# Performance work log

Measured on AMD Instinct MI355X. Metric: run time of the kernel, lower is better.

## Reference

```python
import jax, jax.numpy as jnp
import numpy as np

N_SEQ, N_RES, C_M = 1024, 768, 64
NUM_HEAD = 8
HEAD_DIM = C_M // NUM_HEAD  # key_dim == value_dim == 8 per head
LARGE = 1e9
LN_EPS = 1e-5
MEAN_EPS = 1e-10


def setup_inputs() -> dict:
    key = jax.random.key(0)
    ks = jax.random.split(key, 8)
    msa_act = jax.random.normal(ks[0], (N_SEQ, N_RES, C_M), dtype=jnp.float32)
    msa_mask = (jax.random.uniform(ks[1], (N_SEQ, N_RES)) > 0.15).astype(jnp.float32)
    # fan-avg uniform init like VarianceScaling(1.0, 'fan_avg', 'uniform')
    def vs(k, shape, fan_in, fan_out):
        limit = jnp.sqrt(3.0 * 2.0 / (fan_in + fan_out))
        return jax.random.uniform(k, shape, minval=-limit, maxval=limit, dtype=jnp.float32)
    return {
        "msa_act": msa_act,
        "msa_mask": msa_mask,
        "ln_scale": jnp.ones((C_M,), jnp.float32),
        "ln_bias": jnp.zeros((C_M,), jnp.float32),
        "query_w": vs(ks[2], (C_M, NUM_HEAD, HEAD_DIM), C_M, NUM_HEAD * HEAD_DIM),
        "key_w": vs(ks[3], (C_M, HEAD_DIM), C_M, HEAD_DIM),
        "value_w": vs(ks[4], (C_M, HEAD_DIM), C_M, HEAD_DIM),
        "gating_w": jnp.zeros((C_M, NUM_HEAD, HEAD_DIM), jnp.float32),
        "gating_b": jnp.ones((NUM_HEAD, HEAD_DIM), jnp.float32),
        "output_w": vs(ks[5], (NUM_HEAD, HEAD_DIM, C_M), NUM_HEAD * HEAD_DIM, C_M),
        "output_b": jnp.zeros((C_M,), jnp.float32),
    }


def reference(msa_act, msa_mask, ln_scale, ln_bias, query_w, key_w, value_w,
              gating_w, gating_b, output_w, output_b):
    # permute: columns become the batch axis b = N_res
    x = jnp.transpose(msa_act, (1, 0, 2))          # [R, S, C]
    mask = jnp.transpose(msa_mask, (1, 0))[..., None]  # [R, S, 1]

    # LayerNorm over channels
    mu = jnp.mean(x, axis=-1, keepdims=True)
    var = jnp.mean(jnp.square(x - mu), axis=-1, keepdims=True)
    x = (x - mu) * jax.lax.rsqrt(var + LN_EPS) * ln_scale + ln_bias

    # shared (non-per-head) K/V projections
    v = jnp.einsum('bka,ac->bkc', x, value_w)      # [R, S, d]
    k = jnp.einsum('bka,ac->bkc', x, key_w)        # [R, S, d]

    # masked-mean single query per column
    q_avg = jnp.sum(mask * x, axis=1) / (jnp.sum(mask, axis=1) + MEAN_EPS)  # [R, C]
    q = jnp.einsum('ba,ahc->bhc', q_avg, query_w) * (HEAD_DIM ** -0.5)      # [R, H, d]

    bias = LARGE * (mask[:, None, :, 0] - 1.0)     # [R, 1, S]
    logits = jnp.einsum('bhc,bkc->bhk', q, k) + bias
    weights = jax.nn.softmax(logits, axis=-1)      # [R, H, S]
    weighted_avg = jnp.einsum('bhk,bkc->bhc', weights, v)  # [R, H, d]

    # sigmoid gating per (query, head, channel)
    gate = jax.nn.sigmoid(jnp.einsum('bqc,chv->bqhv', x, gating_w) + gating_b)  # [R, S, H, d]
    gated = weighted_avg[:, None] * gate           # [R, S, H, d]
    out = jnp.einsum('bqhc,hco->bqo', gated, output_w) + output_b  # [R, S, C]

    return jnp.transpose(out, (1, 0, 2))           # [S, R, C]
```

## Files before the change

kernel.cpp:

```cpp
#include <hip/hip_runtime.h>
#include <hip/hip_bf16.h>

#define N_S 1024
#define N_R 768
#define LN_EPS 1e-5f
#define MEAN_EPS 1e-10f
#define LARGE_F 1e9f
#define QSCALE 0.35355339059327373f

typedef __attribute__((ext_vector_type(8))) __bf16 bf16x8;
typedef __attribute__((ext_vector_type(4))) float f32x4;

__device__ __forceinline__ float bflo(unsigned u){ union{unsigned v; float f;} x; x.v = u << 16; return x.f; }
__device__ __forceinline__ unsigned short f2b(float f){
  __hip_bfloat16 h = __float2bfloat16(f);
  return *reinterpret_cast<unsigned short*>(&h);
}
__device__ __forceinline__ unsigned pk2(float a, float b){
  return (unsigned)f2b(a) | ((unsigned)f2b(b) << 16);
}
__device__ __forceinline__ bf16x8 ld_frag(const void* p){
  uint4 u = *reinterpret_cast<const uint4*>(p);
  return __builtin_bit_cast(bf16x8, u);
}

__device__ __forceinline__ void weight_prep(int wave, int lane,
    const float* __restrict__ gw, const float* __restrict__ ow, uint4* __restrict__ wsf)
{
  #pragma unroll 1
  for (int rep = 0; rep < 2; rep++) {
    int fi = wave + rep * 4;
    int mf = fi >> 1, ks = fi & 1;
    int g = lane >> 4, c15 = lane & 15;
    union { uint4 u; unsigned short h[8]; } ghi, glo, ohi, olo;
    #pragma unroll
    for (int t = 0; t < 8; t++) {
      int k = ks * 32 + g * 8 + t;
      float gv = gw[k * 64 + mf * 16 + c15];
      unsigned short gh = f2b(gv);
      ghi.h[t] = gh;
      glo.h[t] = f2b(gv - bflo(gh));
      float ov = ow[k * 64 + mf * 16 + c15];
      unsigned short oh = f2b(ov);
      ohi.h[t] = oh;
      olo.h[t] = f2b(ov - bflo(oh));
    }
    wsf[(0 * 8 + fi) * 64 + lane] = ghi.u;
    wsf[(1 * 8 + fi) * 64 + lane] = glo.u;
    wsf[(2 * 8 + fi) * 64 + lane] = ohi.u;
    wsf[(3 * 8 + fi) * 64 + lane] = olo.u;
  }
}

__global__ __launch_bounds__(256, 2) void lnkv_kernel(
    const float* __restrict__ act, const float* __restrict__ mask,
    const float* __restrict__ lns, const float* __restrict__ lnb,
    const float* __restrict__ kw,  const float* __restrict__ vw,
    const float* __restrict__ gw,  const float* __restrict__ ow,
    _Float16* __restrict__ kvws,   float* __restrict__ qpart,
    float* __restrict__ mpart,     uint4* __restrict__ wsf)
{
  __shared__ float redA[4][64];
  __shared__ float redB[4];

  const int tid  = threadIdx.x;
  const int lane = tid & 63;
  const int wave = tid >> 6;
  const int b    = blockIdx.x;

  if (b >= 6144) { weight_prep(wave, lane, gw, ow, wsf); return; }

  const int r  = b >> 3;
  const int sc = b & 7;
  const int s  = sc * 128 + (tid >> 1);
  const int h  = tid & 1;

  float rw[32];
  {
    const float4* rp = reinterpret_cast<const float4*>(
        act + ((size_t)s * N_R + r) * 64 + h * 32);
    #pragma unroll
    for (int i = 0; i < 8; i++) reinterpret_cast<float4*>(rw)[i] = rp[i];
  }
  float m = mask[(size_t)s * N_R + r];

  float sum = 0.f, ss = 0.f;
  #pragma unroll
  for (int i = 0; i < 32; i++) { sum += rw[i]; ss += rw[i] * rw[i]; }
  sum += __shfl_xor(sum, 1);
  ss  += __shfl_xor(ss, 1);
  float mu  = sum * (1.f / 64.f);
  float rsd = rsqrtf(ss * (1.f / 64.f) - mu * mu + LN_EPS);

  float kacc[8], vacc[8];
  #pragma unroll
  for (int d = 0; d < 8; d++) { kacc[d] = 0.f; vacc[d] = 0.f; }
  #pragma unroll
  for (int i = 0; i < 32; i++) {
    int c = h * 32 + i;
    float xn = fmaf((rw[i] - mu) * rsd, lns[c], lnb[c]);
    rw[i] = m * xn;
    #pragma unroll
    for (int d = 0; d < 8; d++) {
      kacc[d] = fmaf(xn, kw[c * 8 + d], kacc[d]);
      vacc[d] = fmaf(xn, vw[c * 8 + d], vacc[d]);
    }
  }
  #pragma unroll
  for (int d = 0; d < 8; d++) {
    kacc[d] += __shfl_xor(kacc[d], 1);
    vacc[d] += __shfl_xor(vacc[d], 1);
  }
  {
    union { uint4 u; _Float16 hh[8]; } pk;
    #pragma unroll
    for (int d = 0; d < 8; d++) pk.hh[d] = (_Float16)(h ? vacc[d] : kacc[d]);
    *reinterpret_cast<uint4*>(kvws + ((size_t)r * N_S + s) * 16 + h * 8) = pk.u;
  }

  #pragma unroll
  for (int half = 16; half >= 1; half >>= 1) {
    const int stride = 32 / half;
    const bool hi = (lane & stride) != 0;
    #pragma unroll
    for (int i = 0; i < half; i++) {
      float gave = hi ? rw[i] : rw[i + half];
      float keep = hi ? rw[i + half] : rw[i];
      rw[i] = keep + __shfl_xor(gave, stride);
    }
  }
  {
    int local = (((lane >> 1) & 1) << 4) | (((lane >> 2) & 1) << 3) |
                (((lane >> 3) & 1) << 2) | (((lane >> 4) & 1) << 1) |
                ((lane >> 5) & 1);
    redA[wave][h * 32 + local] = rw[0];
  }
  float ms = h ? 0.f : m;
  #pragma unroll
  for (int o = 32; o > 0; o >>= 1) ms += __shfl_xor(ms, o);
  if (lane == 0) redB[wave] = ms;
  __syncthreads();
  if (tid < 64)
    qpart[((size_t)sc * N_R + r) * 64 + tid] =
        redA[0][tid] + redA[1][tid] + redA[2][tid] + redA[3][tid];
  if (tid == 64)
    mpart[sc * N_R + r] = redB[0] + redB[1] + redB[2] + redB[3];
}

__global__ __launch_bounds__(256, 2) void softmax_kernel(
    const float* __restrict__ mask, const float* __restrict__ qpart,
    const float* __restrict__ mpart, const float* __restrict__ qw,
    const _Float16* __restrict__ kvws, float* __restrict__ wavg_out)
{
  __shared__ float redA[4][64];
  __shared__ float redB[4][8];
  __shared__ float q_lds[64];
  __shared__ float qf_lds[64];

  const int tid  = threadIdx.x;
  const int lane = tid & 63;
  const int wave = tid >> 6;
  const int r    = blockIdx.x;

  if (tid < 64) {
    float qs = 0.f;
    #pragma unroll
    for (int p = 0; p < 8; p++) qs += qpart[((size_t)p * N_R + r) * 64 + tid];
    float mt = 0.f;
    #pragma unroll
    for (int p = 0; p < 8; p++) mt += mpart[p * N_R + r];
    q_lds[tid] = qs / (mt + MEAN_EPS);
  }
  __syncthreads();
  if (tid < 64) {
    float acc = 0.f;
    for (int c = 0; c < 64; c++) acc = fmaf(q_lds[c], qw[c * 64 + tid], acc);
    qf_lds[tid] = acc * QSCALE;
  }
  __syncthreads();

  float qreg[64];
  #pragma unroll
  for (int j = 0; j < 64; j++) qreg[j] = qf_lds[j];

  float ev[4][8];
  float hm[8];
  #pragma unroll
  for (int h = 0; h < 8; h++) hm[h] = -1e30f;

  #pragma unroll
  for (int it = 0; it < 4; it++) {
    int s = tid + it * 256;
    union { uint4 u; _Float16 h[8]; } kb;
    kb.u = *reinterpret_cast<const uint4*>(kvws + ((size_t)r * N_S + s) * 16);
    float kk[8];
    #pragma unroll
    for (int d = 0; d < 8; d++) kk[d] = (float)kb.h[d];
    float m = mask[(size_t)s * N_R + r];
    float bias = LARGE_F * (m - 1.f);
    #pragma unroll
    for (int h = 0; h < 8; h++) {
      float l = bias;
      #pragma unroll
      for (int d = 0; d < 8; d++) l = fmaf(qreg[h * 8 + d], kk[d], l);
      ev[it][h] = l;
      hm[h] = fmaxf(hm[h], l);
    }
  }
  #pragma unroll
  for (int h = 0; h < 8; h++) {
    #pragma unroll
    for (int o = 32; o > 0; o >>= 1) hm[h] = fmaxf(hm[h], __shfl_xor(hm[h], o));
  }
  if (lane == 0) {
    #pragma unroll
    for (int h = 0; h < 8; h++) redB[wave][h] = hm[h];
  }
  __syncthreads();
  #pragma unroll
  for (int h = 0; h < 8; h++)
    hm[h] = fmaxf(fmaxf(redB[0][h], redB[1][h]), fmaxf(redB[2][h], redB[3][h]));
  __syncthreads();

  float hs[8];
  #pragma unroll
  for (int h = 0; h < 8; h++) hs[h] = 0.f;
  #pragma unroll
  for (int it = 0; it < 4; it++) {
    #pragma unroll
    for (int h = 0; h < 8; h++) {
      float e = __expf(ev[it][h] - hm[h]);
      ev[it][h] = e;
      hs[h] += e;
    }
  }
  #pragma unroll
  for (int h = 0; h < 8; h++) {
    #pragma unroll
    for (int o = 32; o > 0; o >>= 1) hs[h] += __shfl_xor(hs[h], o);
  }
  if (lane == 0) {
    #pragma unroll
    for (int h = 0; h < 8; h++) redB[wave][h] = hs[h];
  }
  __syncthreads();

  float wacc[64];
  #pragma unroll
  for (int j = 0; j < 64; j++) wacc[j] = 0.f;
  #pragma unroll
  for (int it = 0; it < 4; it++) {
    int s = tid + it * 256;
    union { uint4 u; _Float16 h[8]; } vb;
    vb.u = *reinterpret_cast<const uint4*>(kvws + ((size_t)r * N_S + s) * 16 + 8);
    float vv[8];
    #pragma unroll
    for (int d = 0; d < 8; d++) vv[d] = (float)vb.h[d];
    #pragma unroll
    for (int h = 0; h < 8; h++) {
      float w = ev[it][h];
      #pragma unroll
      for (int d = 0; d < 8; d++) wacc[h * 8 + d] = fmaf(w, vv[d], wacc[h * 8 + d]);
    }
  }
  #pragma unroll
  for (int j = 0; j < 64; j++) {
    #pragma unroll
    for (int o = 32; o > 0; o >>= 1) wacc[j] += __shfl_xor(wacc[j], o);
  }
  if (lane == 0) {
    #pragma unroll
    for (int j = 0; j < 64; j++) redA[wave][j] = wacc[j];
  }
  __syncthreads();
  if (tid < 64) {
    int h = tid >> 3;
    float hsv = redB[0][h] + redB[1][h] + redB[2][h] + redB[3][h];
    wavg_out[r * 64 + tid] =
        (redA[0][tid] + redA[1][tid] + redA[2][tid] + redA[3][tid]) / hsv;
  }
}

struct SharedS { _Float16 kv[N_S][16]; };

__global__ __launch_bounds__(256, 2) void stats_kernel(
    const float* __restrict__ act, const float* __restrict__ mask,
    const float* __restrict__ lns, const float* __restrict__ lnb,
    const float* __restrict__ qw,  const float* __restrict__ kw,
    const float* __restrict__ vw,  const float* __restrict__ gw,
    const float* __restrict__ ow,  float* __restrict__ wavg_out,
    uint4* __restrict__ wsf)
{
  __shared__ SharedS sh;
  __shared__ float redA[4][64];
  __shared__ float redB[4][8];
  __shared__ float q_lds[64];
  __shared__ float qf_lds[64];

  const int tid  = threadIdx.x;
  const int lane = tid & 63;
  const int wave = tid >> 6;
  const int r    = blockIdx.x;

  if (r >= N_R) { weight_prep(wave, lane, gw, ow, wsf); return; }

  float qacc[64];
  #pragma unroll
  for (int c = 0; c < 64; c++) qacc[c] = 0.f;
  float msum = 0.f;

  #pragma unroll 1
  for (int it = 0; it < 4; it++) {
    int s = tid + it * 256;
    size_t base = ((size_t)s * N_R + r) * 64;
    float rw[64];
    const float4* rp = reinterpret_cast<const float4*>(act + base);
    #pragma unroll
    for (int i = 0; i < 16; i++) reinterpret_cast<float4*>(rw)[i] = rp[i];
    float m = mask[(size_t)s * N_R + r];
    float sum = 0.f, ss = 0.f;
    #pragma unroll
    for (int c = 0; c < 64; c++) { sum += rw[c]; ss += rw[c] * rw[c]; }
    float mu  = sum * (1.f / 64.f);
    float rsd = rsqrtf(ss * (1.f / 64.f) - mu * mu + LN_EPS);
    float kacc[8], vacc[8];
    #pragma unroll
    for (int d = 0; d < 8; d++) { kacc[d] = 0.f; vacc[d] = 0.f; }
    #pragma unroll
    for (int c = 0; c < 64; c++) {
      float xn = fmaf((rw[c] - mu) * rsd, lns[c], lnb[c]);
      qacc[c] = fmaf(m, xn, qacc[c]);
      #pragma unroll
      for (int d = 0; d < 8; d++) {
        kacc[d] = fmaf(xn, kw[c * 8 + d], kacc[d]);
        vacc[d] = fmaf(xn, vw[c * 8 + d], vacc[d]);
      }
    }
    union { uint4 u; _Float16 h[8]; } kb, vb;
    #pragma unroll
    for (int d = 0; d < 8; d++) { kb.h[d] = (_Float16)kacc[d]; vb.h[d] = (_Float16)vacc[d]; }
    *reinterpret_cast<uint4*>(&sh.kv[s][0]) = kb.u;
    *reinterpret_cast<uint4*>(&sh.kv[s][8]) = vb.u;
    msum += m;
  }

  #pragma unroll
  for (int c = 0; c < 64; c++) {
    #pragma unroll
    for (int o = 32; o > 0; o >>= 1) qacc[c] += __shfl_xor(qacc[c], o);
  }
  #pragma unroll
  for (int o = 32; o > 0; o >>= 1) msum += __shfl_xor(msum, o);
  if (lane == 0) {
    redB[wave][0] = msum;
    #pragma unroll
    for (int c = 0; c < 64; c++) redA[wave][c] = qacc[c];
  }
  __syncthreads();
  if (tid < 64) {
    float qs = redA[0][tid] + redA[1][tid] + redA[2][tid] + redA[3][tid];
    float mt = redB[0][0] + redB[1][0] + redB[2][0] + redB[3][0];
    q_lds[tid] = qs / (mt + MEAN_EPS);
  }
  __syncthreads();
  if (tid < 64) {
    float acc = 0.f;
    for (int c = 0; c < 64; c++) acc = fmaf(q_lds[c], qw[c * 64 + tid], acc);
    qf_lds[tid] = acc * QSCALE;
  }
  __syncthreads();

  float qreg[64];
  #pragma unroll
  for (int j = 0; j < 64; j++) qreg[j] = qf_lds[j];
  float ev[4][8];
  float hm[8];
  #pragma unroll
  for (int h = 0; h < 8; h++) hm[h] = -1e30f;
  #pragma unroll
  for (int it = 0; it < 4; it++) {
    int s = tid + it * 256;
    union { uint4 u; _Float16 h[8]; } kb;
    kb.u = *reinterpret_cast<uint4*>(&sh.kv[s][0]);
    float kk[8];
    #pragma unroll
    for (int d = 0; d < 8; d++) kk[d] = (float)kb.h[d];
    float m = mask[(size_t)s * N_R + r];
    float bias = LARGE_F * (m - 1.f);
    #pragma unroll
    for (int h = 0; h < 8; h++) {
      float l = bias;
      #pragma unroll
      for (int d = 0; d < 8; d++) l = fmaf(qreg[h * 8 + d], kk[d], l);
      ev[it][h] = l;
      hm[h] = fmaxf(hm[h], l);
    }
  }
  #pragma unroll
  for (int h = 0; h < 8; h++) {
    #pragma unroll
    for (int o = 32; o > 0; o >>= 1) hm[h] = fmaxf(hm[h], __shfl_xor(hm[h], o));
  }
  if (lane == 0) {
    #pragma unroll
    for (int h = 0; h < 8; h++) redB[wave][h] = hm[h];
  }
  __syncthreads();
  #pragma unroll
  for (int h = 0; h < 8; h++)
    hm[h] = fmaxf(fmaxf(redB[0][h], redB[1][h]), fmaxf(redB[2][h], redB[3][h]));
  __syncthreads();

  float hs[8];
  #pragma unroll
  for (int h = 0; h < 8; h++) hs[h] = 0.f;
  #pragma unroll
  for (int it = 0; it < 4; it++) {
    #pragma unroll
    for (int h = 0; h < 8; h++) {
      float e = __expf(ev[it][h] - hm[h]);
      ev[it][h] = e;
      hs[h] += e;
    }
  }
  #pragma unroll
  for (int h = 0; h < 8; h++) {
    #pragma unroll
    for (int o = 32; o > 0; o >>= 1) hs[h] += __shfl_xor(hs[h], o);
  }
  if (lane == 0) {
    #pragma unroll
    for (int h = 0; h < 8; h++) redB[wave][h] = hs[h];
  }
  __syncthreads();

  float wacc[64];
  #pragma unroll
  for (int j = 0; j < 64; j++) wacc[j] = 0.f;
  #pragma unroll
  for (int it = 0; it < 4; it++) {
    int s = tid + it * 256;
    union { uint4 u; _Float16 h[8]; } vb;
    vb.u = *reinterpret_cast<uint4*>(&sh.kv[s][8]);
    float vv[8];
    #pragma unroll
    for (int d = 0; d < 8; d++) vv[d] = (float)vb.h[d];
    #pragma unroll
    for (int h = 0; h < 8; h++) {
      float w = ev[it][h];
      #pragma unroll
      for (int d = 0; d < 8; d++) wacc[h * 8 + d] = fmaf(w, vv[d], wacc[h * 8 + d]);
    }
  }
  #pragma unroll
  for (int j = 0; j < 64; j++) {
    #pragma unroll
    for (int o = 32; o > 0; o >>= 1) wacc[j] += __shfl_xor(wacc[j], o);
  }
  if (lane == 0) {
    #pragma unroll
    for (int j = 0; j < 64; j++) redA[wave][j] = wacc[j];
  }
  __syncthreads();
  if (tid < 64) {
    int h = tid >> 3;
    float hsv = redB[0][h] + redB[1][h] + redB[2][h] + redB[3][h];
    wavg_out[r * 64 + tid] =
        (redA[0][tid] + redA[1][tid] + redA[2][tid] + redA[3][tid]) / hsv;
  }
}

__device__ __forceinline__ void proj_tile(
    const float4 (&rv)[4], int t, int wv, int lane, int qr, int qc, int g, int c15,
    const float* __restrict__ lns, const float* __restrict__ lnb,
    const float* __restrict__ gb, const float* __restrict__ ob,
    const float* __restrict__ wavg, const uint4 (*wfrag)[64],
    char* my, float* __restrict__ out)
{
  const int r  = t >> 4;
  const int s0 = ((t & 15) << 6) + wv * 16;

  float sum = 0.f, ssq = 0.f;
  #pragma unroll
  for (int i = 0; i < 4; i++) {
    sum += rv[i].x + rv[i].y + rv[i].z + rv[i].w;
    ssq += rv[i].x * rv[i].x + rv[i].y * rv[i].y + rv[i].z * rv[i].z + rv[i].w * rv[i].w;
  }
  sum += __shfl_xor(sum, 1); ssq += __shfl_xor(ssq, 1);
  sum += __shfl_xor(sum, 2); ssq += __shfl_xor(ssq, 2);
  float mu  = sum * (1.f / 64.f);
  float rsd = rsqrtf(ssq * (1.f / 64.f) - mu * mu + LN_EPS);

  #pragma unroll
  for (int i = 0; i < 4; i++) {
    int c0 = 16 * i + 4 * qc;
    float4 s4 = *reinterpret_cast<const float4*>(lns + c0);
    float4 b4 = *reinterpret_cast<const float4*>(lnb + c0);
    float x0 = fmaf((rv[i].x - mu) * rsd, s4.x, b4.x);
    float x1 = fmaf((rv[i].y - mu) * rsd, s4.y, b4.y);
    float x2 = fmaf((rv[i].z - mu) * rsd, s4.z, b4.z);
    float x3 = fmaf((rv[i].w - mu) * rsd, s4.w, b4.w);
    uint2 p; p.x = pk2(x0, x1); p.y = pk2(x2, x3);
    int byt = ((2 * i + (qc >> 1)) << 8) + (qr << 4) + ((qc & 1) << 3);
    *reinterpret_cast<uint2*>(my + byt) = p;
  }
  asm volatile("" ::: "memory");
  bf16x8 xb0 = ld_frag(my + lane * 16);
  bf16x8 xb1 = ld_frag(my + 1024 + lane * 16);

  const f32x4 zero = {0.f, 0.f, 0.f, 0.f};
  f32x4 acc[4] = {zero, zero, zero, zero};
  #pragma unroll
  for (int mf = 0; mf < 4; mf++) {
    acc[mf] = __builtin_amdgcn_mfma_f32_16x16x32_bf16(ld_frag(&wfrag[     mf*2    ][lane]), xb0, acc[mf], 0, 0, 0);
    acc[mf] = __builtin_amdgcn_mfma_f32_16x16x32_bf16(ld_frag(&wfrag[ 8 + mf*2    ][lane]), xb0, acc[mf], 0, 0, 0);
    acc[mf] = __builtin_amdgcn_mfma_f32_16x16x32_bf16(ld_frag(&wfrag[     mf*2 + 1][lane]), xb1, acc[mf], 0, 0, 0);
    acc[mf] = __builtin_amdgcn_mfma_f32_16x16x32_bf16(ld_frag(&wfrag[ 8 + mf*2 + 1][lane]), xb1, acc[mf], 0, 0, 0);
  }

  asm volatile("" ::: "memory");
  #pragma unroll
  for (int mf = 0; mf < 4; mf++) {
    int jb = mf * 16 + 4 * g;
    float4 wv4 = *reinterpret_cast<const float4*>(wavg + r * 64 + jb);
    float4 gb4 = *reinterpret_cast<const float4*>(gb + jb);
    float c0 = wv4.x / (1.f + __expf(-(acc[mf][0] + gb4.x)));
    float c1 = wv4.y / (1.f + __expf(-(acc[mf][1] + gb4.y)));
    float c2 = wv4.z / (1.f + __expf(-(acc[mf][2] + gb4.z)));
    float c3 = wv4.w / (1.f + __expf(-(acc[mf][3] + gb4.w)));
    uint2 p; p.x = pk2(c0, c1); p.y = pk2(c2, c3);
    int byt = ((2 * mf + (g >> 1)) << 8) + (c15 << 4) + ((g & 1) << 3);
    *reinterpret_cast<uint2*>(my + byt) = p;
  }
  asm volatile("" ::: "memory");
  bf16x8 cb0 = ld_frag(my + lane * 16);
  bf16x8 cb1 = ld_frag(my + 1024 + lane * 16);

  f32x4 acc2[4] = {zero, zero, zero, zero};
  #pragma unroll
  for (int mf = 0; mf < 4; mf++) {
    acc2[mf] = __builtin_amdgcn_mfma_f32_16x16x32_bf16(ld_frag(&wfrag[16 + mf*2    ][lane]), cb0, acc2[mf], 0, 0, 0);
    acc2[mf] = __builtin_amdgcn_mfma_f32_16x16x32_bf16(ld_frag(&wfrag[24 + mf*2    ][lane]), cb0, acc2[mf], 0, 0, 0);
    acc2[mf] = __builtin_amdgcn_mfma_f32_16x16x32_bf16(ld_frag(&wfrag[16 + mf*2 + 1][lane]), cb1, acc2[mf], 0, 0, 0);
    acc2[mf] = __builtin_amdgcn_mfma_f32_16x16x32_bf16(ld_frag(&wfrag[24 + mf*2 + 1][lane]), cb1, acc2[mf], 0, 0, 0);
  }

  size_t obase = ((size_t)(s0 + c15) * N_R + r) * 64;
  #pragma unroll
  for (int mf = 0; mf < 4; mf++) {
    int o0 = mf * 16 + 4 * g;
    float4 e = *reinterpret_cast<const float4*>(ob + o0);
    float4 o4;
    o4.x = acc2[mf][0] + e.x;
    o4.y = acc2[mf][1] + e.y;
    o4.z = acc2[mf][2] + e.z;
    o4.w = acc2[mf][3] + e.w;
    *reinterpret_cast<float4*>(out + obase + o0) = o4;
  }
}

__global__ __launch_bounds__(256, 4) void proj_kernel(
    const float* __restrict__ act, const float* __restrict__ lns,
    const float* __restrict__ lnb, const float* __restrict__ gb,
    const float* __restrict__ ob,  const float* __restrict__ wavg,
    const uint4* __restrict__ wsf, float* __restrict__ out)
{
  __shared__ uint4 wfrag[32][64];
  __shared__ __align__(16) char wbuf[4][2048];

  const int tid  = threadIdx.x;
  const int lane = tid & 63;
  const int wv   = tid >> 6;
  const int b    = blockIdx.x;
  const int qr = lane >> 2, qc = lane & 3;
  const int g = lane >> 4, c15 = lane & 15;
  char* my = wbuf[wv];

  float4 rvA[4], rvB[4];
  {
    int t = b;
    const float4* ap = reinterpret_cast<const float4*>(
        act + ((size_t)((((t & 15) << 6) + wv * 16) + qr) * N_R + (t >> 4)) * 64);
    rvA[0] = ap[qc]; rvA[1] = ap[qc + 4]; rvA[2] = ap[qc + 8]; rvA[3] = ap[qc + 12];
  }
  {
    uint4* dst = &wfrag[0][0];
    #pragma unroll
    for (int i = 0; i < 8; i++) dst[tid + i * 256] = wsf[tid + i * 256];
  }
  __syncthreads();

  #pragma unroll 1
  for (int i = 0; i < 12; i += 2) {
    {
      int t = (i + 1) * 1024 + b;
      const float4* ap = reinterpret_cast<const float4*>(
          act + ((size_t)((((t & 15) << 6) + wv * 16) + qr) * N_R + (t >> 4)) * 64);
      rvB[0] = ap[qc]; rvB[1] = ap[qc + 4]; rvB[2] = ap[qc + 8]; rvB[3] = ap[qc + 12];
    }
    proj_tile(rvA, i * 1024 + b, wv, lane, qr, qc, g, c15, lns, lnb, gb, ob, wavg, wfrag, my, out);
    if (i + 2 < 12) {
      int t = (i + 2) * 1024 + b;
      const float4* ap = reinterpret_cast<const float4*>(
          act + ((size_t)((((t & 15) << 6) + wv * 16) + qr) * N_R + (t >> 4)) * 64);
      rvA[0] = ap[qc]; rvA[1] = ap[qc + 4]; rvA[2] = ap[qc + 8]; rvA[3] = ap[qc + 12];
    }
    proj_tile(rvB, (i + 1) * 1024 + b, wv, lane, qr, qc, g, c15, lns, lnb, gb, ob, wavg, wfrag, my, out);
  }
}

extern "C" void kernel_launch(void* const* d_in, const int* in_sizes, int n_in,
                              void* d_out, int out_size, void* d_ws, size_t ws_size,
                              hipStream_t stream)
{
  const float* act  = (const float*)d_in[0];
  const float* mask = (const float*)d_in[1];
  const float* lns  = (const float*)d_in[2];
  const float* lnb  = (const float*)d_in[3];
  const float* qw   = (const float*)d_in[4];
  const float* kw   = (const float*)d_in[5];
  const float* vw   = (const float*)d_in[6];
  const float* gw   = (const float*)d_in[7];
  const float* gb   = (const float*)d_in[8];
  const float* ow   = (const float*)d_in[9];
  const float* ob   = (const float*)d_in[10];

  char* ws = (char*)d_ws;
  float* wavg_ws = (float*)ws;
  uint4* wsf     = (uint4*)(ws + 196608);
  const size_t OFF_KV = 229376;
  const size_t OFF_QP = OFF_KV + 25165824;
  const size_t OFF_MP = OFF_QP + 1572864;
  const size_t NEED   = OFF_MP + 24576;

  if (ws_size >= NEED) {
    _Float16* kvws = (_Float16*)(ws + OFF_KV);
    float* qpart   = (float*)(ws + OFF_QP);
    float* mpart   = (float*)(ws + OFF_MP);
    lnkv_kernel<<<6145, 256, 0, stream>>>(act, mask, lns, lnb, kw, vw, gw, ow,
                                          kvws, qpart, mpart, wsf);
    softmax_kernel<<<N_R, 256, 0, stream>>>(mask, qpart, mpart, qw, kvws, wavg_ws);
  } else {
    stats_kernel<<<N_R + 1, 256, 0, stream>>>(act, mask, lns, lnb, qw, kw, vw,
                                              gw, ow, wavg_ws, wsf);
  }
  proj_kernel<<<1024, 256, 0, stream>>>(act, lns, lnb, gb, ob,
                                        wavg_ws, (const uint4*)wsf, (float*)d_out);
}
```

Before: 662.3 us.

## Cache normalized activations as bf16 MFMA fragments and restructure LN/KV pass

The LN/KV pass is reorganized so each thread handles a full 64-channel row, and blocks cover 16 residues by 32 sequences. When the workspace is large enough, it also writes the normalized activations as bf16 MFMA-ready fragments. A new projection kernel then reads these fragments directly, so it no longer re-reads fp32 activations and recomputes LayerNorm. The mask sum moves into the softmax kernel, which removes the mpart buffer. The trade-off is a roughly 100 MB workspace write plus read and bf16 rounding of the normalized input, depending on whether the workspace exceeds the new threshold.

```diff
diff --git a/kernel.cpp b/kernel.cpp
--- a/kernel.cpp
+++ b/kernel.cpp
@@ -52,108 +52,142 @@
   }
 }
 
-__global__ __launch_bounds__(256, 2) void lnkv_kernel(
+template<bool BIG>
+__global__ __launch_bounds__(256, 2) void lnkv2_kernel(
     const float* __restrict__ act, const float* __restrict__ mask,
     const float* __restrict__ lns, const float* __restrict__ lnb,
     const float* __restrict__ kw,  const float* __restrict__ vw,
     const float* __restrict__ gw,  const float* __restrict__ ow,
     _Float16* __restrict__ kvws,   float* __restrict__ qpart,
-    float* __restrict__ mpart,     uint4* __restrict__ wsf)
+    uint4* __restrict__ xnf,       uint4* __restrict__ wsf)
 {
-  __shared__ float redA[4][64];
-  __shared__ float redB[4];
+  __shared__ float wsum[4][16][64];
 
   const int tid  = threadIdx.x;
   const int lane = tid & 63;
   const int wave = tid >> 6;
   const int b    = blockIdx.x;
 
-  if (b >= 6144) { weight_prep(wave, lane, gw, ow, wsf); return; }
-
-  const int r  = b >> 3;
-  const int sc = b & 7;
-  const int s  = sc * 128 + (tid >> 1);
-  const int h  = tid & 1;
-
-  float rw[32];
+  if (b >= 1536) { weight_prep(wave, lane, gw, ow, wsf); return; }
+
+  const int rcb = b >> 5;
+  const int sc  = b & 31;
+  const int r0  = rcb * 16;
+  const int rl  = lane & 15;
+  const int sl  = tid >> 4;
+  const int r   = r0 + rl;
+  const int chA = (((lane >> 5) & 1) << 4) | (((lane >> 4) & 1) << 5);
+
+  float qacc[16];
+  #pragma unroll
+  for (int i = 0; i < 16; i++) qacc[i] = 0.f;
+
+  #pragma unroll 1
+  for (int k = 0; k < 2; k++) {
+    const int s = sc * 32 + sl * 2 + k;
+    const size_t rowbase = ((size_t)s * N_R + r) * 64;
+
+    float rw[64];
+    {
+      const float4* rp = reinterpret_cast<const float4*>(act + rowbase);
+      #pragma unroll
+      for (int i = 0; i < 16; i++) reinterpret_cast<float4*>(rw)[i] = rp[i];
+    }
+    float m = mask[(size_t)s * N_R + r];
+
+    float sum = 0.f, ss = 0.f;
+    #pragma unroll
+    for (int c = 0; c < 64; c++) { sum += rw[c]; ss += rw[c] * rw[c]; }
+    float mu  = sum * (1.f / 64.f);
+    float rsd = rsqrtf(ss * (1.f / 64.f) - mu * mu + LN_EPS);
+
+    float kacc[8], vacc[8];
+    #pragma unroll
+    for (int d = 0; d < 8; d++) { kacc[d] = 0.f; vacc[d] = 0.f; }
+    #pragma unroll
+    for (int c = 0; c < 64; c++) {
+      float xn = fmaf((rw[c] - mu) * rsd, lns[c], lnb[c]);
+      rw[c] = xn;
+      #pragma unroll
+      for (int d = 0; d < 8; d++) {
+        kacc[d] = fmaf(xn, kw[c * 8 + d], kacc[d]);
+        vacc[d] = fmaf(xn, vw[c * 8 + d], vacc[d]);
+      }
+    }
+    {
+      union { uint4 u; _Float16 hh[8]; } kb, vb;
+      #pragma unroll
+      for (int d = 0; d < 8; d++) { kb.hh[d] = (_Float16)kacc[d]; vb.hh[d] = (_Float16)vacc[d]; }
+      _Float16* kvp = kvws + ((size_t)r * N_S + s) * 16;
+      *reinterpret_cast<uint4*>(kvp)     = kb.u;
+      *reinterpret_cast<uint4*>(kvp + 8) = vb.u;
+    }
+
+    if (BIG) {
+      const size_t tb = ((size_t)rcb * 1024 + s) * 128;
+      #pragma unroll
+      for (int oct = 0; oct < 8; oct++) {
+        uint4 w;
+        w.x = pk2(rw[oct * 8 + 0], rw[oct * 8 + 1]);
+        w.y = pk2(rw[oct * 8 + 2], rw[oct * 8 + 3]);
+        w.z = pk2(rw[oct * 8 + 4], rw[oct * 8 + 5]);
+        w.w = pk2(rw[oct * 8 + 6], rw[oct * 8 + 7]);
+        xnf[tb + (oct >> 2) * 64 + (oct & 3) * 16 + rl] = w;
+      }
+    }
+
+    #pragma unroll
+    for (int c = 0; c < 64; c++) rw[c] *= m;
+    {
+      const bool hi = (lane & 16) != 0;
+      #pragma unroll
+      for (int i = 0; i < 32; i++) {
+        float gave = hi ? rw[i] : rw[i + 32];
+        float keep = hi ? rw[i + 32] : rw[i];
+        rw[i] = keep + __shfl_xor(gave, 16);
+      }
+    }
+    {
+      const bool hi = (lane & 32) != 0;
+      #pragma unroll
+      for (int i = 0; i < 16; i++) {
+        float gave = hi ? rw[i] : rw[i + 16];
+        float keep = hi ? rw[i + 16] : rw[i];
+        rw[i] = keep + __shfl_xor(gave, 32);
+      }
+    }
+    #pragma unroll
+    for (int i = 0; i < 16; i++) qacc[i] += rw[i];
+  }
+
+  #pragma unroll
+  for (int i = 0; i < 16; i++) wsum[wave][rl][i + chA] = qacc[i];
+  __syncthreads();
+
   {
-    const float4* rp = reinterpret_cast<const float4*>(
-        act + ((size_t)s * N_R + r) * 64 + h * 32);
-    #pragma unroll
-    for (int i = 0; i < 8; i++) reinterpret_cast<float4*>(rw)[i] = rp[i];
-  }
-  float m = mask[(size_t)s * N_R + r];
-
-  float sum = 0.f, ss = 0.f;
-  #pragma unroll
-  for (int i = 0; i < 32; i++) { sum += rw[i]; ss += rw[i] * rw[i]; }
-  sum += __shfl_xor(sum, 1);
-  ss  += __shfl_xor(ss, 1);
-  float mu  = sum * (1.f / 64.f);
-  float rsd = rsqrtf(ss * (1.f / 64.f) - mu * mu + LN_EPS);
-
-  float kacc[8], vacc[8];
-  #pragma unroll
-  for (int d = 0; d < 8; d++) { kacc[d] = 0.f; vacc[d] = 0.f; }
-  #pragma unroll
-  for (int i = 0; i < 32; i++) {
-    int c = h * 32 + i;
-    float xn = fmaf((rw[i] - mu) * rsd, lns[c], lnb[c]);
-    rw[i] = m * xn;
-    #pragma unroll
-    for (int d = 0; d < 8; d++) {
-      kacc[d] = fmaf(xn, kw[c * 8 + d], kacc[d]);
-      vacc[d] = fmaf(xn, vw[c * 8 + d], vacc[d]);
-    }
-  }
-  #pragma unroll
-  for (int d = 0; d < 8; d++) {
-    kacc[d] += __shfl_xor(kacc[d], 1);
-    vacc[d] += __shfl_xor(vacc[d], 1);
-  }
-  {
-    union { uint4 u; _Float16 hh[8]; } pk;
-    #pragma unroll
-    for (int d = 0; d < 8; d++) pk.hh[d] = (_Float16)(h ? vacc[d] : kacc[d]);
-    *reinterpret_cast<uint4*>(kvws + ((size_t)r * N_S + s) * 16 + h * 8) = pk.u;
-  }
-
-  #pragma unroll
-  for (int half = 16; half >= 1; half >>= 1) {
-    const int stride = 32 / half;
-    const bool hi = (lane & stride) != 0;
-    #pragma unroll
-    for (int i = 0; i < half; i++) {
-      float gave = hi ? rw[i] : rw[i + half];
-      float keep = hi ? rw[i + half] : rw[i];
-      rw[i] = keep + __shfl_xor(gave, stride);
-    }
-  }
-  {
-    int local = (((lane >> 1) & 1) << 4) | (((lane >> 2) & 1) << 3) |
-                (((lane >> 3) & 1) << 2) | (((lane >> 4) & 1) << 1) |
-                ((lane >> 5) & 1);
-    redA[wave][h * 32 + local] = rw[0];
-  }
-  float ms = h ? 0.f : m;
-  #pragma unroll
-  for (int o = 32; o > 0; o >>= 1) ms += __shfl_xor(ms, o);
-  if (lane == 0) redB[wave] = ms;
-  __syncthreads();
-  if (tid < 64)
-    qpart[((size_t)sc * N_R + r) * 64 + tid] =
-        redA[0][tid] + redA[1][tid] + redA[2][tid] + redA[3][tid];
-  if (tid == 64)
-    mpart[sc * N_R + r] = redB[0] + redB[1] + redB[2] + redB[3];
-}
-
-__global__ __launch_bounds__(256, 2) void softmax_kernel(
+    const int rl2 = tid >> 4;
+    const int c0  = (tid & 15) * 4;
+    float4 a = *reinterpret_cast<const float4*>(&wsum[0][rl2][c0]);
+    float4 b1 = *reinterpret_cast<const float4*>(&wsum[1][rl2][c0]);
+    float4 c1 = *reinterpret_cast<const float4*>(&wsum[2][rl2][c0]);
+    float4 d1 = *reinterpret_cast<const float4*>(&wsum[3][rl2][c0]);
+    float4 o;
+    o.x = a.x + b1.x + c1.x + d1.x;
+    o.y = a.y + b1.y + c1.y + d1.y;
+    o.z = a.z + b1.z + c1.z + d1.z;
+    o.w = a.w + b1.w + c1.w + d1.w;
+    *reinterpret_cast<float4*>(&qpart[((size_t)sc * N_R + r0 + rl2) * 64 + c0]) = o;
+  }
+}
+
+__global__ __launch_bounds__(256, 2) void softmax2_kernel(
     const float* __restrict__ mask, const float* __restrict__ qpart,
-    const float* __restrict__ mpart, const float* __restrict__ qw,
-    const _Float16* __restrict__ kvws, float* __restrict__ wavg_out)
+    const float* __restrict__ qw,   const _Float16* __restrict__ kvws,
+    float* __restrict__ wavg_out)
 {
   __shared__ float redA[4][64];
   __shared__ float redB[4][8];
+  __shared__ float redM[4];
   __shared__ float q_lds[64];
   __shared__ float qf_lds[64];
 
@@ -162,13 +196,21 @@
   const int wave = tid >> 6;
   const int r    = blockIdx.x;
 
+  float mreg[4];
+  #pragma unroll
+  for (int it = 0; it < 4; it++) mreg[it] = mask[(size_t)(tid + it * 256) * N_R + r];
+  {
+    float ms = mreg[0] + mreg[1] + mreg[2] + mreg[3];
+    #pragma unroll
+    for (int o = 32; o > 0; o >>= 1) ms += __shfl_xor(ms, o);
+    if (lane == 0) redM[wave] = ms;
+  }
+  __syncthreads();
   if (tid < 64) {
     float qs = 0.f;
-    #pragma unroll
-    for (int p = 0; p < 8; p++) qs += qpart[((size_t)p * N_R + r) * 64 + tid];
-    float mt = 0.f;
-    #pragma unroll
-    for (int p = 0; p < 8; p++) mt += mpart[p * N_R + r];
+    #pragma unroll 1
+    for (int p = 0; p < 32; p++) qs += qpart[((size_t)p * N_R + r) * 64 + tid];
+    float mt = redM[0] + redM[1] + redM[2] + redM[3];
     q_lds[tid] = qs / (mt + MEAN_EPS);
   }
   __syncthreads();
@@ -196,8 +238,7 @@
     float kk[8];
     #pragma unroll
     for (int d = 0; d < 8; d++) kk[d] = (float)kb.h[d];
-    float m = mask[(size_t)s * N_R + r];
-    float bias = LARGE_F * (m - 1.f);
+    float bias = LARGE_F * (mreg[it] - 1.f);
     #pragma unroll
     for (int h = 0; h < 8; h++) {
       float l = bias;
@@ -278,6 +319,92 @@
     float hsv = redB[0][h] + redB[1][h] + redB[2][h] + redB[3][h];
     wavg_out[r * 64 + tid] =
         (redA[0][tid] + redA[1][tid] + redA[2][tid] + redA[3][tid]) / hsv;
+  }
+}
+
+__global__ __launch_bounds__(256, 4) void proj2_kernel(
+    const uint4* __restrict__ xnf, const float* __restrict__ gb,
+    const float* __restrict__ ob,  const float* __restrict__ wavg,
+    const uint4* __restrict__ wsf, float* __restrict__ out)
+{
+  __shared__ uint4 wfrag[32][64];
+  __shared__ __align__(16) char wbuf[4][2048];
+
+  const int tid  = threadIdx.x;
+  const int lane = tid & 63;
+  const int wv   = tid >> 6;
+  const int b    = blockIdx.x;
+  const int g = lane >> 4, c15 = lane & 15;
+  char* my = wbuf[wv];
+
+  {
+    uint4* dst = &wfrag[0][0];
+    #pragma unroll
+    for (int i = 0; i < 8; i++) dst[tid + i * 256] = wsf[tid + i * 256];
+  }
+  __syncthreads();
+
+  const f32x4 zero = {0.f, 0.f, 0.f, 0.f};
+
+  #pragma unroll 1
+  for (int i = 0; i < 12; i++) {
+    const int t  = i * 4096 + b * 4 + wv;
+    const int rc = t >> 10, s = t & 1023;
+    const int r0 = rc << 4;
+    const uint4* tb = xnf + (size_t)t * 128;
+
+    bf16x8 xb0 = ld_frag(tb + lane);
+    bf16x8 xb1 = ld_frag(tb + 64 + lane);
+
+    f32x4 acc[4] = {zero, zero, zero, zero};
+    #pragma unroll
+    for (int mf = 0; mf < 4; mf++) {
+      acc[mf] = __builtin_amdgcn_mfma_f32_16x16x32_bf16(ld_frag(&wfrag[     mf*2    ][lane]), xb0, acc[mf], 0, 0, 0);
+      acc[mf] = __builtin_amdgcn_mfma_f32_16x16x32_bf16(ld_frag(&wfrag[ 8 + mf*2    ][lane]), xb0, acc[mf], 0, 0, 0);
+      acc[mf] = __builtin_amdgcn_mfma_f32_16x16x32_bf16(ld_frag(&wfrag[     mf*2 + 1][lane]), xb1, acc[mf], 0, 0, 0);
+      acc[mf] = __builtin_amdgcn_mfma_f32_16x16x32_bf16(ld_frag(&wfrag[ 8 + mf*2 + 1][lane]), xb1, acc[mf], 0, 0, 0);
+    }
+
+    asm volatile("" ::: "memory");
+    #pragma unroll
+    for (int mf = 0; mf < 4; mf++) {
+      int jb = mf * 16 + 4 * g;
+      float4 wv4 = *reinterpret_cast<const float4*>(wavg + (r0 + c15) * 64 + jb);
+      float4 gb4 = *reinterpret_cast<const float4*>(gb + jb);
+      float c0 = wv4.x / (1.f + __expf(-(acc[mf][0] + gb4.x)));
+      float c1 = wv4.y / (1.f + __expf(-(acc[mf][1] + gb4.y)));
+      float c2 = wv4.z / (1.f + __expf(-(acc[mf][2] + gb4.z)));
+      float c3 = wv4.w / (1.f + __expf(-(acc[mf][3] + gb4.w)));
+      uint2 p; p.x = pk2(c0, c1); p.y = pk2(c2, c3);
+      int byt = ((2 * mf + (g >> 1)) << 8) + (c15 << 4) + ((g & 1) << 3);
+      *reinterpret_cast<uint2*>(my + byt) = p;
+    }
+    asm volatile("" ::: "memory");
+    bf16x8 cb0 = ld_frag(my + lane * 16);
+    bf16x8 cb1 = ld_frag(my + 1024 + lane * 16);
+
+    f32x4 acc2[4] = {zero, zero, zero, zero};
+    #pragma unroll
+    for (int mf = 0; mf < 4; mf++) {
+      acc2[mf] = __builtin_amdgcn_mfma_f32_16x16x32_bf16(ld_frag(&wfrag[16 + mf*2    ][lane]), cb0, acc2[mf], 0, 0, 0);
+      acc2[mf] = __builtin_amdgcn_mfma_f32_16x16x32_bf16(ld_frag(&wfrag[24 + mf*2    ][lane]), cb0, acc2[mf], 0, 0, 0);
+      acc2[mf] = __builtin_amdgcn_mfma_f32_16x16x32_bf16(ld_frag(&wfrag[16 + mf*2 + 1][lane]), cb1, acc2[mf], 0, 0, 0);
+      acc2[mf] = __builtin_amdgcn_mfma_f32_16x16x32_bf16(ld_frag(&wfrag[24 + mf*2 + 1][lane]), cb1, acc2[mf], 0, 0, 0);
+    }
+
+    asm volatile("" ::: "memory");
+    const size_t obase = ((size_t)s * N_R + r0 + c15) * 64;
+    #pragma unroll
+    for (int mf = 0; mf < 4; mf++) {
+      int o0 = mf * 16 + 4 * g;
+      float4 e = *reinterpret_cast<const float4*>(ob + o0);
+      float4 o4;
+      o4.x = acc2[mf][0] + e.x;
+      o4.y = acc2[mf][1] + e.y;
+      o4.z = acc2[mf][2] + e.z;
+      o4.w = acc2[mf][3] + e.w;
+      *reinterpret_cast<float4*>(out + obase + o0) = o4;
+    }
   }
 }
 
@@ -628,22 +755,33 @@
   char* ws = (char*)d_ws;
   float* wavg_ws = (float*)ws;
   uint4* wsf     = (uint4*)(ws + 196608);
-  const size_t OFF_KV = 229376;
-  const size_t OFF_QP = OFF_KV + 25165824;
-  const size_t OFF_MP = OFF_QP + 1572864;
-  const size_t NEED   = OFF_MP + 24576;
-
-  if (ws_size >= NEED) {
+  const size_t OFF_KV  = 229376;
+  const size_t OFF_QP  = OFF_KV + 25165824;
+  const size_t OFF_XNF = OFF_QP + 6291456;
+  const size_t NEED_MID = OFF_XNF;
+  const size_t NEED_BIG = OFF_XNF + 100663296;
+
+  if (ws_size >= NEED_MID) {
     _Float16* kvws = (_Float16*)(ws + OFF_KV);
     float* qpart   = (float*)(ws + OFF_QP);
-    float* mpart   = (float*)(ws + OFF_MP);
-    lnkv_kernel<<<6145, 256, 0, stream>>>(act, mask, lns, lnb, kw, vw, gw, ow,
-                                          kvws, qpart, mpart, wsf);
-    softmax_kernel<<<N_R, 256, 0, stream>>>(mask, qpart, mpart, qw, kvws, wavg_ws);
+    uint4* xnf     = (uint4*)(ws + OFF_XNF);
+    if (ws_size >= NEED_BIG) {
+      lnkv2_kernel<true><<<1537, 256, 0, stream>>>(act, mask, lns, lnb, kw, vw, gw, ow,
+                                                   kvws, qpart, xnf, wsf);
+      softmax2_kernel<<<N_R, 256, 0, stream>>>(mask, qpart, qw, kvws, wavg_ws);
+      proj2_kernel<<<1024, 256, 0, stream>>>(xnf, gb, ob, wavg_ws,
+                                             (const uint4*)wsf, (float*)d_out);
+    } else {
+      lnkv2_kernel<false><<<1537, 256, 0, stream>>>(act, mask, lns, lnb, kw, vw, gw, ow,
+                                                    kvws, qpart, xnf, wsf);
+      softmax2_kernel<<<N_R, 256, 0, stream>>>(mask, qpart, qw, kvws, wavg_ws);
+      proj_kernel<<<1024, 256, 0, stream>>>(act, lns, lnb, gb, ob,
+                                            wavg_ws, (const uint4*)wsf, (float*)d_out);
+    }
   } else {
     stats_kernel<<<N_R + 1, 256, 0, stream>>>(act, mask, lns, lnb, qw, kw, vw,
                                               gw, ow, wavg_ws, wsf);
-  }
-  proj_kernel<<<1024, 256, 0, stream>>>(act, lns, lnb, gb, ob,
-                                        wavg_ws, (const uint4*)wsf, (float*)d_out);
-}
+    proj_kernel<<<1024, 256, 0, stream>>>(act, lns, lnb, gb, ob,
+                                          wavg_ws, (const uint4*)wsf, (float*)d_out);
+  }
+}
```

After: 574.6 us. 13.2% less time.
